# Performance work log

Hardware: AMD Instinct MI355X
Metric: run time of the kernel (lower is better)

The kernel has to match this reference:

```python
import jax, jax.numpy as jnp
import numpy as np

NU, NM, E, L = 100000, 20000, 3200000, 1000000
FD, H = 128, 64


def setup_inputs() -> dict:
    key = jax.random.key(0)
    ks = jax.random.split(key, 32)
    s = 0.05
    inp = {
        'movie_x': jax.random.normal(ks[0], (NM, FD), jnp.float32),
        'edge_src_user': jax.random.randint(ks[1], (E,), 0, NU),
        'edge_dst_movie': jax.random.randint(ks[2], (E,), 0, NM),
        'label_user': jax.random.randint(ks[3], (L,), 0, NU),
        'label_movie': jax.random.randint(ks[4], (L,), 0, NM),
        'user_emb': jax.random.normal(ks[5], (NU, H), jnp.float32) * s,
        'proj_w': jax.random.normal(ks[6], (FD, H), jnp.float32) * s,
        'proj_b': jnp.zeros((H,), jnp.float32),
        'dec_w1': jax.random.normal(ks[7], (2 * H, H), jnp.float32) * s,
        'dec_b1': jnp.zeros((H,), jnp.float32),
        'dec_w2': jax.random.normal(ks[8], (H, 1), jnp.float32) * s,
        'dec_b2': jnp.zeros((1,), jnp.float32),
    }
    i = 9
    for layer in ('1', '2'):
        for rel in ('um', 'mu'):
            inp[f'w{layer}_{rel}_l'] = jax.random.normal(ks[i], (H, H), jnp.float32) * s; i += 1
            inp[f'b{layer}_{rel}_l'] = jnp.zeros((H,), jnp.float32)
            inp[f'w{layer}_{rel}_r'] = jax.random.normal(ks[i], (H, H), jnp.float32) * s; i += 1
    return inp


def _sage(x_src, x_dst, e_src, e_dst, n_dst, w_l, b_l, w_r):
    # PyG SAGEConv, aggr='mean': out = lin_l(mean_j x_src[j]) + lin_r(x_dst)
    msg = x_src[e_src]                                      # [E, H] gather
    agg = jax.ops.segment_sum(msg, e_dst, num_segments=n_dst)
    cnt = jax.ops.segment_sum(jnp.ones((e_dst.shape[0],), x_src.dtype), e_dst, num_segments=n_dst)
    agg = agg / jnp.maximum(cnt, 1.0)[:, None]
    return agg @ w_l + b_l + x_dst @ w_r


def reference(movie_x, edge_src_user, edge_dst_movie, label_user, label_movie,
              user_emb, proj_w, proj_b,
              w1_um_l, b1_um_l, w1_um_r, w1_mu_l, b1_mu_l, w1_mu_r,
              w2_um_l, b2_um_l, w2_um_r, w2_mu_l, b2_mu_l, w2_mu_r,
              dec_w1, dec_b1, dec_w2, dec_b2):
    nu, nm = user_emb.shape[0], movie_x.shape[0]
    user0 = user_emb
    movie0 = movie_x @ proj_w + proj_b
    # conv1 (user->movie and movie->user), then ReLU
    movie1 = jax.nn.relu(_sage(user0, movie0, edge_src_user, edge_dst_movie, nm, w1_um_l, b1_um_l, w1_um_r))
    user1 = jax.nn.relu(_sage(movie0, user0, edge_dst_movie, edge_src_user, nu, w1_mu_l, b1_mu_l, w1_mu_r))
    # conv2 (no activation)
    movie2 = _sage(user1, movie1, edge_src_user, edge_dst_movie, nm, w2_um_l, b2_um_l, w2_um_r)
    user2 = _sage(movie1, user1, edge_dst_movie, edge_src_user, nu, w2_mu_l, b2_mu_l, w2_mu_r)
    # edge decoder: gather -> concat -> MLP
    x = jnp.concatenate([user2[label_user], movie2[label_movie]], axis=-1)  # [L, 2H]
    x = jax.nn.relu(x @ dec_w1 + dec_b1)
    return x @ dec_w2 + dec_b2
```

## Files before the change

kernel.cpp:

```cpp
#include <hip/hip_runtime.h>

static constexpr int NU = 100000;
static constexpr int NM = 20000;
static constexpr int NE = 3200000;
static constexpr int NL = 1000000;
static constexpr int FD = 128;
static constexpr int H  = 64;

static constexpr int MBK = 16;
static constexpr int UBK = 64;
static constexpr int NBM = NM / MBK;
static constexpr int NBU = (NU + UBK - 1) / UBK;
static constexpr int CAP_M = 4096;
static constexpr int CAP_U = 3072;
static constexpr int B2C = 8192;

typedef __attribute__((ext_vector_type(8))) short short8v;
typedef __attribute__((ext_vector_type(4))) float f32x4;

__device__ __forceinline__ ushort bf16rne(float x) {
  unsigned u = __float_as_uint(x);
  return (ushort)((u + 0x7fffu + ((u >> 16) & 1u)) >> 16);
}

__global__ void k_binit2(int* __restrict__ bcur_m, int* __restrict__ bcur_u) {
  int i = blockIdx.x * 256 + threadIdx.x;
  if (i < NBM) bcur_m[i] = i * CAP_M;
  if (i < NBU) bcur_u[i] = i * CAP_U;
}

__global__ void __launch_bounds__(256) k_bin2(
    const int* __restrict__ esrc, const int* __restrict__ edst,
    int* __restrict__ bcur_m, int* __restrict__ bcur_u,
    unsigned* __restrict__ pairs_m, unsigned* __restrict__ pairs_u, int nbPerSide) {
  __shared__ unsigned stage[B2C];
  __shared__ int cnt[NBU];
  __shared__ int lofs[NBU];
  __shared__ int gbase[NBU];
  __shared__ int wpart[4];
  int tid = threadIdx.x;
  bool um = (int)blockIdx.x < nbPerSide;
  int cb = um ? blockIdx.x : blockIdx.x - nbPerSide;
  int nbs = um ? NBM : NBU;
  int* bcur = um ? bcur_m : bcur_u;
  unsigned* pairs = um ? pairs_m : pairs_u;
  int e0 = cb * B2C, e1 = min(e0 + B2C, NE);
  for (int i = tid; i < nbs; i += 256) cnt[i] = 0;
  __syncthreads();
  for (int e = e0 + tid; e < e1; e += 256) {
    int key = um ? edst[e] : esrc[e];
    int b = um ? (key >> 4) : (key >> 6);
    atomicAdd(&cnt[b], 1);
  }
  __syncthreads();
  int PT = (nbs + 255) / 256;
  int lo = tid * PT, hi = min(lo + PT, nbs);
  int run = 0;
  for (int i = lo; i < hi; ++i) { lofs[i] = run; run += cnt[i]; }
  int part = run;
  int lane = tid & 63, wid = tid >> 6;
  int v = part;
  #pragma unroll
  for (int off = 1; off < 64; off <<= 1) {
    int t = __shfl_up(v, off, 64);
    if (lane >= off) v += t;
  }
  if (lane == 63) wpart[wid] = v;
  __syncthreads();
  int woff = 0;
  for (int wj = 0; wj < wid; ++wj) woff += wpart[wj];
  int excl = woff + v - part;
  for (int i = lo; i < hi; ++i) {
    lofs[i] += excl;
    int c = cnt[i];
    gbase[i] = (c > 0) ? atomicAdd(&bcur[i], c) : 0;
    cnt[i] = 0;
  }
  __syncthreads();
  for (int e = e0 + tid; e < e1; e += 256) {
    int s = esrc[e], d = edst[e];
    if (um) {
      int b = d >> 4;
      int r = atomicAdd(&cnt[b], 1);
      stage[lofs[b] + r] = ((unsigned)d << 17) | (unsigned)s;
    } else {
      int b = s >> 6;
      int r = atomicAdd(&cnt[b], 1);
      stage[lofs[b] + r] = ((unsigned)s << 15) | (unsigned)d;
    }
  }
  __syncthreads();
  int ne = e1 - e0;
  for (int slot = tid; slot < ne; slot += 256) {
    unsigned v2 = stage[slot];
    int b = um ? ((int)(v2 >> 17) >> 4) : ((int)(v2 >> 15) >> 6);
    pairs[gbase[b] + (slot - lofs[b])] = v2 & 0x1FFFFFu;
  }
}

__global__ void __launch_bounds__(256) k_sortb4(
    const unsigned* __restrict__ pairs_m, const unsigned* __restrict__ pairs_u,
    const int* __restrict__ bcur_m, const int* __restrict__ bcur_u,
    int* __restrict__ st_m, int* __restrict__ dg_m, int* __restrict__ out_m,
    int* __restrict__ st_u, int* __restrict__ dg_u, int* __restrict__ out_u) {
  __shared__ int cnt[64];
  __shared__ int cbase[64];
  const unsigned* pairs; const int* bcur; int* start; int* deg; int* out_idx;
  int b, npb, shift, cap, n; unsigned mask;
  if ((int)blockIdx.x < NBM) {
    pairs = pairs_m; bcur = bcur_m; start = st_m; deg = dg_m; out_idx = out_m;
    b = blockIdx.x; npb = MBK; shift = 17; mask = 0x1FFFFu; cap = CAP_M; n = NM;
  } else {
    pairs = pairs_u; bcur = bcur_u; start = st_u; deg = dg_u; out_idx = out_u;
    b = blockIdx.x - NBM; npb = UBK; shift = 15; mask = 0x7FFFu; cap = CAP_U; n = NU;
  }
  int tid = threadIdx.x;
  if (tid < 64) cnt[tid] = 0;
  __syncthreads();
  int e0 = b * cap, e1 = bcur[b];
  for (int e = e0 + tid; e < e1; e += 256) atomicAdd(&cnt[pairs[e] >> shift], 1);
  __syncthreads();
  if (tid < 64) {
    int c = cnt[tid];
    int v = c;
    #pragma unroll
    for (int off = 1; off < 64; off <<= 1) {
      int t = __shfl_up(v, off, 64);
      if (tid >= off) v += t;
    }
    int basee = e0 + v - c;
    cbase[tid] = basee;
    int node = b * npb + tid;
    if (tid < npb && node < n) { start[node] = basee; deg[node] = c; }
    cnt[tid] = 0;
  }
  __syncthreads();
  for (int e = e0 + tid; e < e1; e += 256) {
    unsigned v = pairs[e];
    int loc = (int)(v >> shift);
    int r = atomicAdd(&cnt[loc], 1);
    out_idx[cbase[loc] + r] = (int)(v & mask);
  }
}

__global__ void __launch_bounds__(256) k_agg2c(
    int gm,
    const ushort* __restrict__ fM, const int* __restrict__ stM, const int* __restrict__ dgM,
    const int* __restrict__ idxM, float* __restrict__ outM, int nM,
    const ushort* __restrict__ fU, const int* __restrict__ stU, const int* __restrict__ dgU,
    const int* __restrict__ idxU, float* __restrict__ outU, int nU) {
  const ushort* feat; const int* st; const int* dg; const int* idxs; float* out; int n, b;
  if ((int)blockIdx.x < gm) { feat = fM; st = stM; dg = dgM; idxs = idxM; out = outM; n = nM; b = blockIdx.x; }
  else { feat = fU; st = stU; dg = dgU; idxs = idxU; out = outU; n = nU; b = blockIdx.x - gm; }
  int lane = threadIdx.x & 63;
  int f4 = lane & 15, p = lane >> 4;
  int d = b * 4 + (threadIdx.x >> 6);
  if (d >= n) return;
  int s = st[d], degn = dg[d];
  int e = s + degn;
  float a0 = 0.f, a1 = 0.f, a2 = 0.f, a3 = 0.f;
  int i = s;
  for (; i + 16 <= e; i += 16) {
    int s0 = idxs[i + 0 + p];
    int s1 = idxs[i + 4 + p];
    int s2 = idxs[i + 8 + p];
    int s3 = idxs[i + 12 + p];
    uint2 v0 = *(const uint2*)(feat + ((size_t)s0 << 6) + (f4 << 2));
    uint2 v1 = *(const uint2*)(feat + ((size_t)s1 << 6) + (f4 << 2));
    uint2 v2 = *(const uint2*)(feat + ((size_t)s2 << 6) + (f4 << 2));
    uint2 v3 = *(const uint2*)(feat + ((size_t)s3 << 6) + (f4 << 2));
    a0 += __uint_as_float(v0.x << 16); a1 += __uint_as_float(v0.x & 0xffff0000u);
    a2 += __uint_as_float(v0.y << 16); a3 += __uint_as_float(v0.y & 0xffff0000u);
    a0 += __uint_as_float(v1.x << 16); a1 += __uint_as_float(v1.x & 0xffff0000u);
    a2 += __uint_as_float(v1.y << 16); a3 += __uint_as_float(v1.y & 0xffff0000u);
    a0 += __uint_as_float(v2.x << 16); a1 += __uint_as_float(v2.x & 0xffff0000u);
    a2 += __uint_as_float(v2.y << 16); a3 += __uint_as_float(v2.y & 0xffff0000u);
    a0 += __uint_as_float(v3.x << 16); a1 += __uint_as_float(v3.x & 0xffff0000u);
    a2 += __uint_as_float(v3.y << 16); a3 += __uint_as_float(v3.y & 0xffff0000u);
  }
  for (; i < e; i += 4) {
    int ii = i + p;
    bool ok = ii < e;
    int sj = idxs[ok ? ii : i];
    uint2 v = *(const uint2*)(feat + ((size_t)sj << 6) + (f4 << 2));
    if (!ok) { v.x = 0u; v.y = 0u; }
    a0 += __uint_as_float(v.x << 16); a1 += __uint_as_float(v.x & 0xffff0000u);
    a2 += __uint_as_float(v.y << 16); a3 += __uint_as_float(v.y & 0xffff0000u);
  }
  a0 += __shfl_xor(a0, 16, 64); a1 += __shfl_xor(a1, 16, 64);
  a2 += __shfl_xor(a2, 16, 64); a3 += __shfl_xor(a3, 16, 64);
  a0 += __shfl_xor(a0, 32, 64); a1 += __shfl_xor(a1, 32, 64);
  a2 += __shfl_xor(a2, 32, 64); a3 += __shfl_xor(a3, 32, 64);
  if (p == 0) {
    float inv = 1.f / fmaxf((float)degn, 1.f);
    float4 o = make_float4(a0 * inv, a1 * inv, a2 * inv, a3 * inv);
    *(float4*)&out[((size_t)d << 6) + (f4 << 2)] = o;
  }
}

__global__ void __launch_bounds__(256) k_proj16(const float* __restrict__ x,
                                                const float* __restrict__ w,
                                                const float* __restrict__ b,
                                                float* __restrict__ out,
                                                ushort* __restrict__ outh) {
  __shared__ float sw[FD * H];
  __shared__ float sx[16][FD];
  int tid = threadIdx.x;
  int r0 = blockIdx.x * 16;
  #pragma unroll
  for (int it = 0; it < 8; ++it) {
    int idx = tid + it * 256;
    ((float4*)sw)[idx] = ((const float4*)w)[idx];
  }
  #pragma unroll
  for (int it = 0; it < 2; ++it) {
    int idx = tid + it * 256;
    int row = idx >> 5, q = idx & 31;
    *(float4*)&sx[row][q * 4] = ((const float4*)x)[(size_t)(r0 + row) * 32 + q];
  }
  __syncthreads();
  int col = tid & 63, rg = tid >> 6;
  float bb = b[col];
  float acc[4];
  #pragma unroll
  for (int j = 0; j < 4; ++j) acc[j] = bb;
  #pragma unroll 4
  for (int k4 = 0; k4 < 32; ++k4) {
    float w0 = sw[(k4 * 4 + 0) * H + col], w1 = sw[(k4 * 4 + 1) * H + col];
    float w2 = sw[(k4 * 4 + 2) * H + col], w3 = sw[(k4 * 4 + 3) * H + col];
    #pragma unroll
    for (int j = 0; j < 4; ++j) {
      float4 a = *(const float4*)&sx[rg + j * 4][k4 * 4];
      acc[j] += a.x * w0 + a.y * w1 + a.z * w2 + a.w * w3;
    }
  }
  #pragma unroll
  for (int j = 0; j < 4; ++j) {
    size_t o = (size_t)(r0 + rg + j * 4) * H + col;
    out[o] = acc[j];
    outh[o] = bf16rne(acc[j]);
  }
}

__global__ void __launch_bounds__(256) k_sage16(
    int gm,
    const float* __restrict__ aggM, const float* __restrict__ xdM,
    const float* __restrict__ wlM, const float* __restrict__ wrM,
    const float* __restrict__ blM, float* __restrict__ outfM, ushort* __restrict__ outhM,
    const float* __restrict__ aggU, const float* __restrict__ xdU,
    const float* __restrict__ wlU, const float* __restrict__ wrU,
    const float* __restrict__ blU, float* __restrict__ outfU, ushort* __restrict__ outhU,
    int relu) {
  __shared__ float swl[H * H];
  __shared__ float swr[H * H];
  __shared__ float sa[16][H];
  __shared__ float sd[16][H];
  int tid = threadIdx.x;
  const float *agg, *xd, *wl, *wr, *bl; float* outf; ushort* outh; int r0;
  if ((int)blockIdx.x < gm) {
    agg = aggM; xd = xdM; wl = wlM; wr = wrM; bl = blM; outf = outfM; outh = outhM;
    r0 = blockIdx.x * 16;
  } else {
    agg = aggU; xd = xdU; wl = wlU; wr = wrU; bl = blU; outf = outfU; outh = outhU;
    r0 = (blockIdx.x - gm) * 16;
  }
  #pragma unroll
  for (int it = 0; it < 4; ++it) {
    int idx = tid + it * 256;
    ((float4*)swl)[idx] = ((const float4*)wl)[idx];
    ((float4*)swr)[idx] = ((const float4*)wr)[idx];
  }
  {
    int row = tid >> 4, q = tid & 15;
    *(float4*)&sa[row][q * 4] = ((const float4*)agg)[(size_t)(r0 + row) * 16 + q];
    *(float4*)&sd[row][q * 4] = ((const float4*)xd)[(size_t)(r0 + row) * 16 + q];
  }
  __syncthreads();
  int col = tid & 63, rg = tid >> 6;
  float b = bl[col];
  float acc[4];
  #pragma unroll
  for (int j = 0; j < 4; ++j) acc[j] = b;
  #pragma unroll 4
  for (int k4 = 0; k4 < 16; ++k4) {
    float w0 = swl[(k4 * 4 + 0) * H + col], w1 = swl[(k4 * 4 + 1) * H + col];
    float w2 = swl[(k4 * 4 + 2) * H + col], w3 = swl[(k4 * 4 + 3) * H + col];
    float v0 = swr[(k4 * 4 + 0) * H + col], v1 = swr[(k4 * 4 + 1) * H + col];
    float v2 = swr[(k4 * 4 + 2) * H + col], v3 = swr[(k4 * 4 + 3) * H + col];
    #pragma unroll
    for (int j = 0; j < 4; ++j) {
      int r = rg + j * 4;
      float4 a = *(const float4*)&sa[r][k4 * 4];
      float4 d = *(const float4*)&sd[r][k4 * 4];
      acc[j] += a.x * w0 + a.y * w1 + a.z * w2 + a.w * w3;
      acc[j] += d.x * v0 + d.y * v1 + d.z * v2 + d.w * v3;
    }
  }
  #pragma unroll
  for (int j = 0; j < 4; ++j) {
    int r = rg + j * 4;
    float v = relu ? fmaxf(acc[j], 0.f) : acc[j];
    size_t o = (size_t)(r0 + r) * H + col;
    if (outf) outf[o] = v;
    if (outh) outh[o] = bf16rne(v);
  }
}

__global__ void __launch_bounds__(256) k_cvtb(const float* __restrict__ src,
                                              ushort* __restrict__ dst, int n4) {
  int i = blockIdx.x * 256 + threadIdx.x;
  if (i >= n4) return;
  float4 v = ((const float4*)src)[i];
  ushort4 o;
  o.x = bf16rne(v.x); o.y = bf16rne(v.y); o.z = bf16rne(v.z); o.w = bf16rne(v.w);
  ((ushort4*)dst)[i] = o;
}

__global__ void k_packw(const float* __restrict__ w1, ushort* __restrict__ pw) {
  int tid = threadIdx.x;
  for (int it = 0; it < 4; ++it) {
    int q = tid + it * 256;
    int kt = q >> 8, ct = (q >> 6) & 3, l = q & 63;
    int kg = l >> 4, cg = l & 15;
    #pragma unroll
    for (int j = 0; j < 8; ++j) {
      int k = kt * 32 + kg * 8 + j;
      int c = ct * 16 + cg;
      float x = w1[k * 64 + c];
      unsigned u = __float_as_uint(x);
      unsigned r = (u + 0x7fffu + ((u >> 16) & 1u)) >> 16;
      float res = x - __uint_as_float(r << 16);
      pw[q * 8 + j] = (ushort)r;
      pw[8192 + q * 8 + j] = (ushort)(__float_as_uint(res) >> 16);
    }
  }
}

__global__ void __launch_bounds__(256) k_dec_mfma(
    const ushort* __restrict__ uhi, const ushort* __restrict__ mhi,
    const int* __restrict__ lu, const int* __restrict__ lm,
    const ushort* __restrict__ pw,
    const float* __restrict__ b1, const float* __restrict__ w2,
    const float* __restrict__ b2, float* __restrict__ out) {
  __shared__ ushort sB[2 * 16 * 64 * 8];
  int tid = threadIdx.x;
  #pragma unroll
  for (int it = 0; it < 8; ++it) {
    int idx = tid + it * 256;
    ((float4*)sB)[idx] = ((const float4*)pw)[idx];
  }
  __syncthreads();
  int l = tid & 63, w = tid >> 6;
  int cg = l & 15, kg = l >> 4;
  float w2f[4], b1f[4];
  #pragma unroll
  for (int ct = 0; ct < 4; ++ct) {
    w2f[ct] = w2[ct * 16 + cg];
    b1f[ct] = b1[ct * 16 + cg];
  }
  float b2v = b2[0];
  for (int t = 0; t < 4; ++t) {
    int Lb = blockIdx.x * 256 + w * 64 + t * 16;
    int lab = min(Lb + cg, NL - 1);
    int nu = lu[lab], nm = lm[lab];
    const size_t ub = (size_t)nu * 64 + kg * 8;
    const size_t mb = (size_t)nm * 64 + kg * 8;
    short8v ah[4];
    ah[0] = *(const short8v*)(uhi + ub);
    ah[1] = *(const short8v*)(uhi + ub + 32);
    ah[2] = *(const short8v*)(mhi + mb);
    ah[3] = *(const short8v*)(mhi + mb + 32);
    f32x4 acc[4];
    #pragma unroll
    for (int ct = 0; ct < 4; ++ct) acc[ct] = (f32x4){b1f[ct], b1f[ct], b1f[ct], b1f[ct]};
    #pragma unroll
    for (int kt = 0; kt < 4; ++kt) {
      #pragma unroll
      for (int ct = 0; ct < 4; ++ct) {
        const int f = kt * 4 + ct;
        short8v bh = *(const short8v*)&sB[(size_t)(f * 64 + l) * 8];
        short8v bl_ = *(const short8v*)&sB[(size_t)((16 + f) * 64 + l) * 8];
        acc[ct] = __builtin_amdgcn_mfma_f32_16x16x32_bf16(ah[kt], bh, acc[ct], 0, 0, 0);
        acc[ct] = __builtin_amdgcn_mfma_f32_16x16x32_bf16(ah[kt], bl_, acc[ct], 0, 0, 0);
      }
    }
    float p[4];
    #pragma unroll
    for (int r = 0; r < 4; ++r) {
      p[r] = fmaxf(acc[0][r], 0.f) * w2f[0] + fmaxf(acc[1][r], 0.f) * w2f[1] +
             fmaxf(acc[2][r], 0.f) * w2f[2] + fmaxf(acc[3][r], 0.f) * w2f[3];
    }
    #pragma unroll
    for (int m = 8; m >= 1; m >>= 1) {
      #pragma unroll
      for (int r = 0; r < 4; ++r) p[r] += __shfl_xor(p[r], m, 64);
    }
    if (cg == 0) {
      #pragma unroll
      for (int r = 0; r < 4; ++r) {
        int row = Lb + kg * 4 + r;
        if (row < NL) out[row] = p[r] + b2v;
      }
    }
  }
}

extern "C" void kernel_launch(void* const* d_in, const int* in_sizes, int n_in,
                              void* d_out, int out_size, void* d_ws, size_t ws_size,
                              hipStream_t stream) {
  const float* movie_x  = (const float*)d_in[0];
  const int*   esrc     = (const int*)d_in[1];
  const int*   edst     = (const int*)d_in[2];
  const int*   lu       = (const int*)d_in[3];
  const int*   lm       = (const int*)d_in[4];
  const float* user_emb = (const float*)d_in[5];
  const float* proj_w   = (const float*)d_in[6];
  const float* proj_b   = (const float*)d_in[7];
  const float* dec_w1   = (const float*)d_in[8];
  const float* dec_b1   = (const float*)d_in[9];
  const float* dec_w2   = (const float*)d_in[10];
  const float* dec_b2   = (const float*)d_in[11];
  const float* w1_um_l  = (const float*)d_in[12];
  const float* b1_um_l  = (const float*)d_in[13];
  const float* w1_um_r  = (const float*)d_in[14];
  const float* w1_mu_l  = (const float*)d_in[15];
  const float* b1_mu_l  = (const float*)d_in[16];
  const float* w1_mu_r  = (const float*)d_in[17];
  const float* w2_um_l  = (const float*)d_in[18];
  const float* b2_um_l  = (const float*)d_in[19];
  const float* w2_um_r  = (const float*)d_in[20];
  const float* w2_mu_l  = (const float*)d_in[21];
  const float* b2_mu_l  = (const float*)d_in[22];
  const float* w2_mu_r  = (const float*)d_in[23];

  char* ws = (char*)d_ws;
  size_t off = 0;
  auto alloc = [&](size_t bytes) {
    void* p = ws + off;
    off = (off + bytes + 255) & ~(size_t)255;
    return p;
  };
  float* movie0   = (float*)alloc((size_t)NM * H * 4);
  float* movie1   = (float*)alloc((size_t)NM * H * 4);
  float* user1    = (float*)alloc((size_t)NU * H * 4);
  float* agg_m    = (float*)alloc((size_t)NM * H * 4);
  float* agg_u    = (float*)alloc((size_t)NU * H * 4);
  unsigned* pairs_m = (unsigned*)user1;
  unsigned* pairs_u = pairs_m + (size_t)NBM * CAP_M;
  ushort* uembh   = (ushort*)alloc((size_t)NU * H * 2);
  ushort* movie0h = (ushort*)alloc((size_t)NM * H * 2);
  ushort* movie1h = (ushort*)alloc((size_t)NM * H * 2);
  ushort* user1h  = (ushort*)alloc((size_t)NU * H * 2);
  ushort* uhi     = (ushort*)alloc((size_t)NU * H * 2);
  ushort* mhi     = (ushort*)alloc((size_t)NM * H * 2);
  int* st_m      = (int*)alloc((size_t)NM * 4);
  int* st_u      = (int*)alloc((size_t)NU * 4);
  int* dg_m      = (int*)alloc((size_t)NM * 4);
  int* dg_u      = (int*)alloc((size_t)NU * 4);
  int* bcur_m    = (int*)alloc((size_t)NBM * 4);
  int* bcur_u    = (int*)alloc((size_t)NBU * 4);
  int* su_by_m   = (int*)alloc((size_t)NBM * CAP_M * 4);
  int* sm_by_u   = (int*)alloc((size_t)NBU * CAP_U * 4);
  ushort* pw     = (ushort*)alloc((size_t)2 * 16 * 64 * 8 * 2);
  (void)ws_size; (void)in_sizes; (void)n_in; (void)out_size;

  k_binit2<<<(NBU + 255) / 256, 256, 0, stream>>>(bcur_m, bcur_u);
  int nbPerSide = (NE + B2C - 1) / B2C;
  k_bin2<<<2 * nbPerSide, 256, 0, stream>>>(esrc, edst, bcur_m, bcur_u,
                                            pairs_m, pairs_u, nbPerSide);
  k_sortb4<<<NBM + NBU, 256, 0, stream>>>(pairs_m, pairs_u, bcur_m, bcur_u,
                                          st_m, dg_m, su_by_m, st_u, dg_u, sm_by_u);

  k_proj16<<<NM / 16, 256, 0, stream>>>(movie_x, proj_w, proj_b, movie0, movie0h);
  k_cvtb<<<(NU * H / 4 + 255) / 256, 256, 0, stream>>>(user_emb, uembh, NU * H / 4);
  k_packw<<<1, 256, 0, stream>>>(dec_w1, pw);

  const int GAM = NM / 4, GAU = NU / 4;
  const int GSM = NM / 16, GSU = NU / 16;

  k_agg2c<<<GAM + GAU, 256, 0, stream>>>(GAM,
      uembh,   st_m, dg_m, su_by_m, agg_m, NM,
      movie0h, st_u, dg_u, sm_by_u, agg_u, NU);
  k_sage16<<<GSM + GSU, 256, 0, stream>>>(GSM,
      agg_m, movie0,   w1_um_l, w1_um_r, b1_um_l, movie1, movie1h,
      agg_u, user_emb, w1_mu_l, w1_mu_r, b1_mu_l, user1,  user1h, 1);

  k_agg2c<<<GAM + GAU, 256, 0, stream>>>(GAM,
      user1h,  st_m, dg_m, su_by_m, agg_m, NM,
      movie1h, st_u, dg_u, sm_by_u, agg_u, NU);
  k_sage16<<<GSM + GSU, 256, 0, stream>>>(GSM,
      agg_m, movie1, w2_um_l, w2_um_r, b2_um_l, (float*)nullptr, mhi,
      agg_u, user1,  w2_mu_l, w2_mu_r, b2_mu_l, (float*)nullptr, uhi, 0);

  k_dec_mfma<<<(NL + 255) / 256, 256, 0, stream>>>(uhi, mhi, lu, lm, pw,
                                                   dec_b1, dec_w2, dec_b2, (float*)d_out);
}
```

Baseline: 520.1 us.

## Vectorize edge binning loads, use 16-bit user-side indices, wider movie aggregation

The binning kernel now reads source and destination indices as int4 vectors, and each block handles a smaller edge chunk so more blocks run. The movie-to-user neighbor index list is stored as ushort, since movie ids fit in 16 bits, which halves that index traffic in both aggregation passes. Movie-side aggregation uses 8 lanes per node with 16-byte loads and 8 neighbors in flight per step, while the user side keeps the 4-wide path. More bin blocks mean more global atomics on the bucket cursors. The int4 loads assume each chunk start is 16-byte aligned, which holds because the chunk size and the edge count are multiples of 4.

Result: slower. 579.9 us (+11.5%).

```diff
diff --git a/kernel.cpp b/kernel.cpp
--- a/kernel.cpp
+++ b/kernel.cpp
@@ -13,7 +13,7 @@
 static constexpr int NBU = (NU + UBK - 1) / UBK;
 static constexpr int CAP_M = 4096;
 static constexpr int CAP_U = 3072;
-static constexpr int B2C = 8192;
+static constexpr int B2C = 4096;
 
 typedef __attribute__((ext_vector_type(8))) short short8v;
 typedef __attribute__((ext_vector_type(4))) float f32x4;
@@ -42,15 +42,19 @@
   bool um = (int)blockIdx.x < nbPerSide;
   int cb = um ? blockIdx.x : blockIdx.x - nbPerSide;
   int nbs = um ? NBM : NBU;
+  int sh = um ? 4 : 6;
   int* bcur = um ? bcur_m : bcur_u;
   unsigned* pairs = um ? pairs_m : pairs_u;
   int e0 = cb * B2C, e1 = min(e0 + B2C, NE);
   for (int i = tid; i < nbs; i += 256) cnt[i] = 0;
   __syncthreads();
-  for (int e = e0 + tid; e < e1; e += 256) {
-    int key = um ? edst[e] : esrc[e];
-    int b = um ? (key >> 4) : (key >> 6);
-    atomicAdd(&cnt[b], 1);
+  const int* keys = um ? edst : esrc;
+  for (int e = e0 + (tid << 2); e < e1; e += 1024) {
+    int4 k = *(const int4*)(keys + e);
+    atomicAdd(&cnt[k.x >> sh], 1);
+    atomicAdd(&cnt[k.y >> sh], 1);
+    atomicAdd(&cnt[k.z >> sh], 1);
+    atomicAdd(&cnt[k.w >> sh], 1);
   }
   __syncthreads();
   int PT = (nbs + 255) / 256;
@@ -77,16 +81,23 @@
     cnt[i] = 0;
   }
   __syncthreads();
-  for (int e = e0 + tid; e < e1; e += 256) {
-    int s = esrc[e], d = edst[e];
-    if (um) {
-      int b = d >> 4;
-      int r = atomicAdd(&cnt[b], 1);
-      stage[lofs[b] + r] = ((unsigned)d << 17) | (unsigned)s;
-    } else {
-      int b = s >> 6;
-      int r = atomicAdd(&cnt[b], 1);
-      stage[lofs[b] + r] = ((unsigned)s << 15) | (unsigned)d;
+  for (int e = e0 + (tid << 2); e < e1; e += 1024) {
+    int4 s4 = *(const int4*)(esrc + e);
+    int4 d4 = *(const int4*)(edst + e);
+    int ss[4] = {s4.x, s4.y, s4.z, s4.w};
+    int dd[4] = {d4.x, d4.y, d4.z, d4.w};
+    #pragma unroll
+    for (int j = 0; j < 4; ++j) {
+      int s = ss[j], d = dd[j];
+      if (um) {
+        int b = d >> 4;
+        int r = atomicAdd(&cnt[b], 1);
+        stage[lofs[b] + r] = ((unsigned)d << 17) | (unsigned)s;
+      } else {
+        int b = s >> 6;
+        int r = atomicAdd(&cnt[b], 1);
+        stage[lofs[b] + r] = ((unsigned)s << 15) | (unsigned)d;
+      }
     }
   }
   __syncthreads();
@@ -102,16 +113,17 @@
     const unsigned* __restrict__ pairs_m, const unsigned* __restrict__ pairs_u,
     const int* __restrict__ bcur_m, const int* __restrict__ bcur_u,
     int* __restrict__ st_m, int* __restrict__ dg_m, int* __restrict__ out_m,
-    int* __restrict__ st_u, int* __restrict__ dg_u, int* __restrict__ out_u) {
+    int* __restrict__ st_u, int* __restrict__ dg_u, ushort* __restrict__ out_u) {
   __shared__ int cnt[64];
   __shared__ int cbase[64];
-  const unsigned* pairs; const int* bcur; int* start; int* deg; int* out_idx;
+  const unsigned* pairs; const int* bcur; int* start; int* deg;
   int b, npb, shift, cap, n; unsigned mask;
-  if ((int)blockIdx.x < NBM) {
-    pairs = pairs_m; bcur = bcur_m; start = st_m; deg = dg_m; out_idx = out_m;
+  bool um = (int)blockIdx.x < NBM;
+  if (um) {
+    pairs = pairs_m; bcur = bcur_m; start = st_m; deg = dg_m;
     b = blockIdx.x; npb = MBK; shift = 17; mask = 0x1FFFFu; cap = CAP_M; n = NM;
   } else {
-    pairs = pairs_u; bcur = bcur_u; start = st_u; deg = dg_u; out_idx = out_u;
+    pairs = pairs_u; bcur = bcur_u; start = st_u; deg = dg_u;
     b = blockIdx.x - NBM; npb = UBK; shift = 15; mask = 0x7FFFu; cap = CAP_U; n = NU;
   }
   int tid = threadIdx.x;
@@ -139,24 +151,65 @@
     unsigned v = pairs[e];
     int loc = (int)(v >> shift);
     int r = atomicAdd(&cnt[loc], 1);
-    out_idx[cbase[loc] + r] = (int)(v & mask);
-  }
-}
-
-__global__ void __launch_bounds__(256) k_agg2c(
-    int gm,
-    const ushort* __restrict__ fM, const int* __restrict__ stM, const int* __restrict__ dgM,
-    const int* __restrict__ idxM, float* __restrict__ outM, int nM,
-    const ushort* __restrict__ fU, const int* __restrict__ stU, const int* __restrict__ dgU,
-    const int* __restrict__ idxU, float* __restrict__ outU, int nU) {
-  const ushort* feat; const int* st; const int* dg; const int* idxs; float* out; int n, b;
-  if ((int)blockIdx.x < gm) { feat = fM; st = stM; dg = dgM; idxs = idxM; out = outM; n = nM; b = blockIdx.x; }
-  else { feat = fU; st = stU; dg = dgU; idxs = idxU; out = outU; n = nU; b = blockIdx.x - gm; }
-  int lane = threadIdx.x & 63;
+    if (um) out_m[cbase[loc] + r] = (int)(v & mask);
+    else    out_u[cbase[loc] + r] = (ushort)(v & mask);
+  }
+}
+
+#define ACC4(vv)                                                           \
+  a0 += __uint_as_float((vv).x << 16); a1 += __uint_as_float((vv).x & 0xffff0000u); \
+  a2 += __uint_as_float((vv).y << 16); a3 += __uint_as_float((vv).y & 0xffff0000u); \
+  a4 += __uint_as_float((vv).z << 16); a5 += __uint_as_float((vv).z & 0xffff0000u); \
+  a6 += __uint_as_float((vv).w << 16); a7 += __uint_as_float((vv).w & 0xffff0000u);
+
+__device__ __forceinline__ void agg_node_w8(const ushort* __restrict__ feat,
+                                            const int* __restrict__ idxs,
+                                            int s, int degn, float* __restrict__ out,
+                                            int d, int lane) {
+  int f8 = lane & 7, p = lane >> 3;
+  int e = s + degn;
+  float a0 = 0.f, a1 = 0.f, a2 = 0.f, a3 = 0.f, a4 = 0.f, a5 = 0.f, a6 = 0.f, a7 = 0.f;
+  int i = s;
+  for (; i + 32 <= e; i += 32) {
+    int s0 = idxs[i + 0 + p];
+    int s1 = idxs[i + 8 + p];
+    int s2 = idxs[i + 16 + p];
+    int s3 = idxs[i + 24 + p];
+    uint4 v0 = *(const uint4*)(feat + ((size_t)s0 << 6) + (f8 << 3));
+    uint4 v1 = *(const uint4*)(feat + ((size_t)s1 << 6) + (f8 << 3));
+    uint4 v2 = *(const uint4*)(feat + ((size_t)s2 << 6) + (f8 << 3));
+    uint4 v3 = *(const uint4*)(feat + ((size_t)s3 << 6) + (f8 << 3));
+    ACC4(v0) ACC4(v1) ACC4(v2) ACC4(v3)
+  }
+  for (; i < e; i += 8) {
+    int ii = i + p;
+    bool ok = ii < e;
+    int sj = idxs[ok ? ii : i];
+    uint4 v = *(const uint4*)(feat + ((size_t)sj << 6) + (f8 << 3));
+    if (!ok) { v.x = 0u; v.y = 0u; v.z = 0u; v.w = 0u; }
+    ACC4(v)
+  }
+  #pragma unroll
+  for (int m = 8; m < 64; m <<= 1) {
+    a0 += __shfl_xor(a0, m, 64); a1 += __shfl_xor(a1, m, 64);
+    a2 += __shfl_xor(a2, m, 64); a3 += __shfl_xor(a3, m, 64);
+    a4 += __shfl_xor(a4, m, 64); a5 += __shfl_xor(a5, m, 64);
+    a6 += __shfl_xor(a6, m, 64); a7 += __shfl_xor(a7, m, 64);
+  }
+  if (p == 0) {
+    float inv = 1.f / fmaxf((float)degn, 1.f);
+    float4 o0 = make_float4(a0 * inv, a1 * inv, a2 * inv, a3 * inv);
+    float4 o1 = make_float4(a4 * inv, a5 * inv, a6 * inv, a7 * inv);
+    *(float4*)&out[((size_t)d << 6) + (f8 << 3)] = o0;
+    *(float4*)&out[((size_t)d << 6) + (f8 << 3) + 4] = o1;
+  }
+}
+
+__device__ __forceinline__ void agg_node_w4(const ushort* __restrict__ feat,
+                                            const ushort* __restrict__ idxs,
+                                            int s, int degn, float* __restrict__ out,
+                                            int d, int lane) {
   int f4 = lane & 15, p = lane >> 4;
-  int d = b * 4 + (threadIdx.x >> 6);
-  if (d >= n) return;
-  int s = st[d], degn = dg[d];
   int e = s + degn;
   float a0 = 0.f, a1 = 0.f, a2 = 0.f, a3 = 0.f;
   int i = s;
@@ -195,6 +248,24 @@
     float inv = 1.f / fmaxf((float)degn, 1.f);
     float4 o = make_float4(a0 * inv, a1 * inv, a2 * inv, a3 * inv);
     *(float4*)&out[((size_t)d << 6) + (f4 << 2)] = o;
+  }
+}
+
+__global__ void __launch_bounds__(256) k_agg2d(
+    int gm,
+    const ushort* __restrict__ fM, const int* __restrict__ stM, const int* __restrict__ dgM,
+    const int* __restrict__ idxM, float* __restrict__ outM, int nM,
+    const ushort* __restrict__ fU, const int* __restrict__ stU, const int* __restrict__ dgU,
+    const ushort* __restrict__ idxU, float* __restrict__ outU, int nU) {
+  int lane = threadIdx.x & 63;
+  if ((int)blockIdx.x < gm) {
+    int d = blockIdx.x * 4 + (threadIdx.x >> 6);
+    if (d >= nM) return;
+    agg_node_w8(fM, idxM, stM[d], dgM[d], outM, d, lane);
+  } else {
+    int d = (blockIdx.x - gm) * 4 + (threadIdx.x >> 6);
+    if (d >= nU) return;
+    agg_node_w4(fU, idxU, stU[d], dgU[d], outU, d, lane);
   }
 }
 
@@ -460,7 +531,7 @@
   int* bcur_m    = (int*)alloc((size_t)NBM * 4);
   int* bcur_u    = (int*)alloc((size_t)NBU * 4);
   int* su_by_m   = (int*)alloc((size_t)NBM * CAP_M * 4);
-  int* sm_by_u   = (int*)alloc((size_t)NBU * CAP_U * 4);
+  ushort* sm_by_u = (ushort*)alloc((size_t)NBU * CAP_U * 2);
   ushort* pw     = (ushort*)alloc((size_t)2 * 16 * 64 * 8 * 2);
   (void)ws_size; (void)in_sizes; (void)n_in; (void)out_size;
 
@@ -478,14 +549,14 @@
   const int GAM = NM / 4, GAU = NU / 4;
   const int GSM = NM / 16, GSU = NU / 16;
 
-  k_agg2c<<<GAM + GAU, 256, 0, stream>>>(GAM,
+  k_agg2d<<<GAM + GAU, 256, 0, stream>>>(GAM,
       uembh,   st_m, dg_m, su_by_m, agg_m, NM,
       movie0h, st_u, dg_u, sm_by_u, agg_u, NU);
   k_sage16<<<GSM + GSU, 256, 0, stream>>>(GSM,
       agg_m, movie0,   w1_um_l, w1_um_r, b1_um_l, movie1, movie1h,
       agg_u, user_emb, w1_mu_l, w1_mu_r, b1_mu_l, user1,  user1h, 1);
 
-  k_agg2c<<<GAM + GAU, 256, 0, stream>>>(GAM,
+  k_agg2d<<<GAM + GAU, 256, 0, stream>>>(GAM,
       user1h,  st_m, dg_m, su_by_m, agg_m, NM,
       movie1h, st_u, dg_u, sm_by_u, agg_u, NU);
   k_sage16<<<GSM + GSU, 256, 0, stream>>>(GSM,
```
